# Kernel optimization log

Hardware: AMD Instinct MI355X
Metric: run time of the kernel (lower is better)

The kernel has to match this reference:

```python
import jax, jax.numpy as jnp
import numpy as np

PROJ_DIM = 128
TEMP = 0.1
CLAMP_VAL = 50.0
EPS = 1e-6


def _coords(H, W):
    # [H*W, 2] grid of (x, y) coordinates, matching torch meshgrid indexing='ij'
    xs = jnp.arange(W, dtype=jnp.float32)
    ys = jnp.arange(H, dtype=jnp.float32)
    grid_y, grid_x = jnp.meshgrid(ys, xs, indexing='ij')
    return jnp.stack([grid_x.reshape(-1), grid_y.reshape(-1)], axis=-1)


def setup_inputs() -> dict:
    key = jax.random.key(0)
    k1, k2 = jax.random.split(key)
    B, C, H, W = 2, 128, 96, 96
    fL = jax.random.normal(k1, (B, C, H, W), dtype=jnp.float32)
    fR = jax.random.normal(k2, (B, C, H, W), dtype=jnp.float32)
    return {"fL": fL, "fR": fR}


def reference(fL, fR):
    B, C, H, W = fL.shape
    HW = H * W
    scale = jnp.float32(np.sqrt(PROJ_DIM))

    # L2-normalize over channel dim with epsilon clamp
    fLn = fL / jnp.maximum(jnp.linalg.norm(fL, axis=1, keepdims=True), EPS)
    fRn = fR / jnp.maximum(jnp.linalg.norm(fR, axis=1, keepdims=True), EPS)

    q = fLn.reshape(B, C, HW).transpose(0, 2, 1).astype(jnp.float32)  # [B, HW, C]
    k = fRn.reshape(B, C, HW).astype(jnp.float32)                      # [B, C, HW]

    coords = _coords(H, W)  # [HW, 2]

    # Global correlation: [B, HW, HW] (chunking in the original is math-equivalent)
    corr = jnp.einsum('bqc,bck->bqk', q, k) / scale
    corr = jnp.clip(corr / TEMP, -CLAMP_VAL, CLAMP_VAL)
    prob = jax.nn.softmax(corr, axis=-1)

    expected_pos = prob @ coords                 # [B, HW, 2]
    max_prob = jnp.max(prob, axis=-1)            # [B, HW]

    flow_abs = expected_pos.reshape(B, H, W, 2).transpose(0, 3, 1, 2)  # [B, 2, H, W]
    conf = max_prob.reshape(B, 1, H, W)

    src = coords.reshape(H, W, 2).transpose(2, 0, 1)[None]  # [1, 2, H, W]
    flow = (flow_abs - src).astype(fL.dtype)
    conf = conf.astype(fL.dtype)
    return flow, conf
```

## Files before the change

### kernel.cpp

```cpp
#include <hip/hip_runtime.h>
#include <stdint.h>

#define HW 9216
#define CDIM 128
#define WIDTH 96
#define BATCH 2
#define SPLITS 4
#define KSPLIT 2304
#define NTILE 18

#define QSCALE 0.44194173824159216f
#define MXSCALE 2.8853900817779268f

typedef _Float16 half8 __attribute__((ext_vector_type(8)));
typedef float f32x16 __attribute__((ext_vector_type(16)));
typedef float float4v __attribute__((ext_vector_type(4)));
typedef float float2v __attribute__((ext_vector_type(2)));

__global__ __launch_bounds__(256) void norm_kernel(const float* __restrict__ fL,
                                                   const float* __restrict__ fR,
                                                   _Float16* __restrict__ Qh,
                                                   _Float16* __restrict__ Kh)
{
    __shared__ float ssred[4][64];
    __shared__ _Float16 ot[64 * 130];

    const float* src = (blockIdx.y == 0) ? fL : fR;
    _Float16* dst    = (blockIdx.y == 0) ? Qh : Kh;
    const float outScale = (blockIdx.y == 0) ? QSCALE : 1.0f;

    const int t = threadIdx.x;
    const int pos_l = t & 63, cg = t >> 6;
    const int pos0 = blockIdx.x * 64;
    const int b = pos0 / HW, pos_in = pos0 % HW + pos_l;

    const float* p = src + (size_t)b * CDIM * HW + pos_in;

    float v[32];
    float ss = 0.f;
    #pragma unroll
    for (int j = 0; j < 32; ++j) {
        v[j] = p[(size_t)(cg * 32 + j) * HW];
        ss += v[j] * v[j];
    }
    ssred[cg][pos_l] = ss;
    __syncthreads();
    float tot = ssred[0][pos_l] + ssred[1][pos_l] + ssred[2][pos_l] + ssred[3][pos_l];
    float scale = outScale / fmaxf(sqrtf(tot), 1e-6f);

    #pragma unroll
    for (int j = 0; j < 32; ++j)
        ot[pos_l * 130 + cg * 32 + j] = (_Float16)(v[j] * scale);
    __syncthreads();

    uint4* og = (uint4*)(dst + (size_t)(b * HW + pos0 % HW + 0) * CDIM);
    #pragma unroll
    for (int i = 0; i < 4; ++i) {
        int idx = i * 256 + t;
        int row = idx >> 4, chunk = idx & 15;
        og[idx] = *(const uint4*)&ot[row * 130 + chunk * 8];
    }
}

__global__ __launch_bounds__(512, 4) void attn_kernel(const _Float16* __restrict__ Qh,
                                                      const _Float16* __restrict__ Kh,
                                                      float4* __restrict__ part)
{
    __shared__ __align__(16) _Float16 Ks[2 * 128 * 128];

    const int qt = blockIdx.x, split = blockIdx.y, b = blockIdx.z;
    const int t = threadIdx.x;
    const int lane = t & 63, wave = t >> 6;
    const int wq = wave >> 2, wk = wave & 3;
    const int lane31 = lane & 31, hi = lane >> 5;
    const int ln15 = lane & 15, qd = lane >> 4;

    const char* kp0 = (const char*)(Kh + (size_t)b * HW * CDIM) +
                      (size_t)(split * KSPLIT) * (CDIM * 2);

    int voff[4];
    #pragma unroll
    for (int i = 0; i < 4; ++i) {
        int r = wave * 16 + i * 4 + qd;
        voff[i] = r * 256 + ((ln15 ^ (r & 15)) << 4);
    }

    #define STAGE(TILE, BUF)                                                     \
        {                                                                        \
            const char* kb_ = kp0 + (size_t)(TILE) * 32768;                      \
            _Float16* db_ = &Ks[(BUF) * 16384 + wave * (16 * 128)];              \
            _Pragma("unroll")                                                    \
            for (int i_ = 0; i_ < 4; ++i_)                                       \
                __builtin_amdgcn_global_load_lds(                                \
                    (const __attribute__((address_space(1))) uint32_t*)(kb_ + voff[i_]), \
                    (__attribute__((address_space(3))) uint32_t*)(db_ + i_ * (4 * 128)), \
                    16, 0, 0);                                                   \
        }

    STAGE(0, 0);

    half8 qf[8];
    {
        const char* qb = (const char*)(Qh +
            ((size_t)(b * HW + qt * 64 + wq * 32 + lane31)) * CDIM);
        #pragma unroll
        for (int kc = 0; kc < 8; ++kc)
            qf[kc] = *(const half8*)(qb + kc * 32 + hi * 16);
    }

    int rdoff[8];
    #pragma unroll
    for (int kc = 0; kc < 8; ++kc)
        rdoff[kc] = ((wk * 32 + lane31) << 8) + ((((kc << 1) | hi) ^ ln15) << 4);

    float2v xb2[3], yw2[3];
    #pragma unroll
    for (int p = 0; p < 3; ++p) {
        xb2[p] = (float2v)(float)(32 * ((p + wk) % 3));
        yw2[p] = (float2v)(float)(split * 24 + (4 * p + wk) / 3);
    }

    float2v E2[8];
    #pragma unroll
    for (int p = 0; p < 8; ++p) E2[p] = (float2v)0.f;
    float2v mx2 = (float2v)(-1.0e30f);
    float2v axb2 = (float2v)0.f, ay2 = (float2v)0.f;

    const char* ksb = (const char*)&Ks[0];
    const float2v C4 = (float2v)(1.0f / 24.0f), C3 = (float2v)(1.0f / 6.0f),
                  C2 = (float2v)0.5f, C1 = (float2v)1.0f;

    __syncthreads();

    #pragma unroll
    for (int kt = 0; kt < NTILE; ++kt) {
        const int cur = kt & 1;
        const int ph = kt % 3;
        const float yadd = (float)(4 * (kt / 3));

        if (kt < NTILE - 1) STAGE(kt + 1, 1 - cur);

        f32x16 acc;
        __builtin_amdgcn_s_setprio(1);
        #pragma unroll
        for (int kc = 0; kc < 8; ++kc) {
            half8 kf = *(const half8*)(ksb + cur * 32768 + rdoff[kc]);
            acc = __builtin_amdgcn_mfma_f32_32x32x16_f16(
                kf, qf[kc], (kc == 0) ? (f32x16)0.f : acc, 0, 0, 0);
        }
        __builtin_amdgcn_s_setprio(0);

        float2v lt2;
        #pragma unroll
        for (int p = 0; p < 8; ++p) {
            float2v w;
            w.x = acc[2 * p];
            w.y = acc[2 * p + 1];
            mx2 = __builtin_elementwise_max(mx2, w);
            float2v h = w * C4 + C3;
            h = h * w + C2;
            h = h * w + C1;
            h = h * w + C1;
            float2v e = h * h;
            E2[p] += e;
            lt2 = (p == 0) ? e : (lt2 + e);
        }
        axb2 += lt2 * xb2[ph];
        ay2  += lt2 * (yw2[ph] + (float2v)yadd);
        __syncthreads();
    }

    float l = 0.f, axc = 0.f;
    #pragma unroll
    for (int p = 0; p < 8; ++p) {
        const float c0 = (float)(((2 * p) & 3) + 8 * ((2 * p) >> 2));
        l   += E2[p].x + E2[p].y;
        axc += c0 * E2[p].x + (c0 + 1.0f) * E2[p].y;
    }
    float ax = axc + (float)(4 * hi) * l + axb2.x + axb2.y;
    float ay = ay2.x + ay2.y;
    float mx = fmaxf(mx2.x, mx2.y);

    l  += __shfl_xor(l, 32, 64);
    ax += __shfl_xor(ax, 32, 64);
    ay += __shfl_xor(ay, 32, 64);
    mx  = fmaxf(mx, __shfl_xor(mx, 32, 64));

    if (hi == 0) {
        int row = qt * 64 + wq * 32 + lane31;
        part[(size_t)(split * 4 + wk) * (BATCH * HW) + b * HW + row] =
            make_float4(l, ax, ay, __builtin_amdgcn_exp2f(mx * MXSCALE));
    }
    #undef STAGE
}

__global__ __launch_bounds__(256) void combine_kernel(const float4* __restrict__ part,
                                                      float* __restrict__ out)
{
    int tid = blockIdx.x * 256 + threadIdx.x;
    int b = tid / HW, pos = tid % HW;
    float l = 0.f, ax = 0.f, ay = 0.f, mx = 0.f;
    #pragma unroll
    for (int s = 0; s < 16; ++s) {
        float4 v = part[(size_t)s * (BATCH * HW) + tid];
        l += v.x; ax += v.y; ay += v.z; mx = fmaxf(mx, v.w);
    }
    float inv = 1.0f / l;
    int x = pos % WIDTH, y = pos / WIDTH;
    out[(size_t)b * 2 * HW + pos]           = ax * inv - (float)x;
    out[(size_t)b * 2 * HW + HW + pos]      = ay * inv - (float)y;
    out[(size_t)BATCH * 2 * HW + (size_t)b * HW + pos] = mx * inv;
}

extern "C" void kernel_launch(void* const* d_in, const int* in_sizes, int n_in,
                              void* d_out, int out_size, void* d_ws, size_t ws_size,
                              hipStream_t stream)
{
    const float* fL = (const float*)d_in[0];
    const float* fR = (const float*)d_in[1];
    float* out = (float*)d_out;

    char* ws = (char*)d_ws;
    const size_t QH_BYTES = (size_t)BATCH * HW * CDIM * sizeof(_Float16);
    _Float16* Qh  = (_Float16*)ws;
    _Float16* Kh  = (_Float16*)(ws + QH_BYTES);
    float4*   part = (float4*)(ws + 2 * QH_BYTES);

    norm_kernel<<<dim3((BATCH * HW) / 64, 2), 256, 0, stream>>>(fL, fR, Qh, Kh);
    attn_kernel<<<dim3(HW / 64, SPLITS, BATCH), 512, 0, stream>>>(Qh, Kh, part);
    combine_kernel<<<dim3((BATCH * HW) / 256), 256, 0, stream>>>(part, out);
}
```

Before: 137.5 us.

## Retile attention to 128-query tiles with triple-buffered K and XCD-aware block mapping

The attention kernel now covers 128 query rows per workgroup (4x2 wave grid) over 64-key tiles instead of 64 queries over 128 keys. This halves how often each K tile is streamed per query and the number of partial results the combine step reduces. K staging moves to a 3-buffer ring that prefetches two tiles ahead, with explicit vmcnt waits and a single barrier per tile in place of two __syncthreads. Blocks are remapped across the 8 XCDs by index swizzling, and launch bounds rise to 6 waves per SIMD. The risks are higher register pressure under the tighter bounds, correctness of the hand-written waitcnt pipeline, and smaller MFMA work per barrier.

```diff
diff --git a/kernel.cpp b/kernel.cpp
--- a/kernel.cpp
+++ b/kernel.cpp
@@ -7,14 +7,16 @@
 #define BATCH 2
 #define SPLITS 4
 #define KSPLIT 2304
-#define NTILE 18
+#define NTILE 36
+#define QTILE 128
+#define NQT (HW / QTILE)
+#define NWG (NQT * SPLITS * BATCH)
 
 #define QSCALE 0.44194173824159216f
 #define MXSCALE 2.8853900817779268f
 
 typedef _Float16 half8 __attribute__((ext_vector_type(8)));
 typedef float f32x16 __attribute__((ext_vector_type(16)));
-typedef float float4v __attribute__((ext_vector_type(4)));
 typedef float float2v __attribute__((ext_vector_type(2)));
 
 __global__ __launch_bounds__(256) void norm_kernel(const float* __restrict__ fL,
@@ -62,35 +64,49 @@
     }
 }
 
-__global__ __launch_bounds__(512, 4) void attn_kernel(const _Float16* __restrict__ Qh,
+__global__ __launch_bounds__(512, 6) void attn_kernel(const _Float16* __restrict__ Qh,
                                                       const _Float16* __restrict__ Kh,
                                                       float4* __restrict__ part)
 {
-    __shared__ __align__(16) _Float16 Ks[2 * 128 * 128];
-
-    const int qt = blockIdx.x, split = blockIdx.y, b = blockIdx.z;
+    __shared__ __align__(16) _Float16 Ks[3 * 64 * 128];
+
+    const int wg0 = blockIdx.x;
+    const int nid = (wg0 & 7) * (NWG / 8) + (wg0 >> 3);
+    const int qt = nid % NQT;
+    const int split = (nid / NQT) % SPLITS;
+    const int b = nid / (NQT * SPLITS);
+
     const int t = threadIdx.x;
     const int lane = t & 63, wave = t >> 6;
-    const int wq = wave >> 2, wk = wave & 3;
+    const int wq = wave >> 1, wk = wave & 1;
     const int lane31 = lane & 31, hi = lane >> 5;
     const int ln15 = lane & 15, qd = lane >> 4;
 
     const char* kp0 = (const char*)(Kh + (size_t)b * HW * CDIM) +
                       (size_t)(split * KSPLIT) * (CDIM * 2);
 
-    int voff[4];
-    #pragma unroll
-    for (int i = 0; i < 4; ++i) {
-        int r = wave * 16 + i * 4 + qd;
+    half8 qf[8];
+    {
+        const char* qb = (const char*)(Qh +
+            ((size_t)(b * HW + qt * QTILE + wq * 32 + lane31)) * CDIM);
+        #pragma unroll
+        for (int kc = 0; kc < 8; ++kc)
+            qf[kc] = *(const half8*)(qb + kc * 32 + hi * 16);
+    }
+
+    int voff[2];
+    #pragma unroll
+    for (int i = 0; i < 2; ++i) {
+        int r = wave * 8 + i * 4 + qd;
         voff[i] = r * 256 + ((ln15 ^ (r & 15)) << 4);
     }
 
     #define STAGE(TILE, BUF)                                                     \
         {                                                                        \
-            const char* kb_ = kp0 + (size_t)(TILE) * 32768;                      \
-            _Float16* db_ = &Ks[(BUF) * 16384 + wave * (16 * 128)];              \
+            const char* kb_ = kp0 + (size_t)(TILE) * 16384;                      \
+            _Float16* db_ = &Ks[(BUF) * 8192 + wave * (8 * 128)];                \
             _Pragma("unroll")                                                    \
-            for (int i_ = 0; i_ < 4; ++i_)                                       \
+            for (int i_ = 0; i_ < 2; ++i_)                                       \
                 __builtin_amdgcn_global_load_lds(                                \
                     (const __attribute__((address_space(1))) uint32_t*)(kb_ + voff[i_]), \
                     (__attribute__((address_space(3))) uint32_t*)(db_ + i_ * (4 * 128)), \
@@ -98,26 +114,18 @@
         }
 
     STAGE(0, 0);
-
-    half8 qf[8];
-    {
-        const char* qb = (const char*)(Qh +
-            ((size_t)(b * HW + qt * 64 + wq * 32 + lane31)) * CDIM);
-        #pragma unroll
-        for (int kc = 0; kc < 8; ++kc)
-            qf[kc] = *(const half8*)(qb + kc * 32 + hi * 16);
-    }
+    STAGE(1, 1);
 
     int rdoff[8];
     #pragma unroll
     for (int kc = 0; kc < 8; ++kc)
         rdoff[kc] = ((wk * 32 + lane31) << 8) + ((((kc << 1) | hi) ^ ln15) << 4);
 
-    float2v xb2[3], yw2[3];
+    float xb[3], yw[3];
     #pragma unroll
     for (int p = 0; p < 3; ++p) {
-        xb2[p] = (float2v)(float)(32 * ((p + wk) % 3));
-        yw2[p] = (float2v)(float)(split * 24 + (4 * p + wk) / 3);
+        xb[p] = (float)(32 * ((2 * p + wk) % 3));
+        yw[p] = (float)(split * 24 + (2 * p + wk) / 3);
     }
 
     float2v E2[8];
@@ -130,21 +138,23 @@
     const float2v C4 = (float2v)(1.0f / 24.0f), C3 = (float2v)(1.0f / 6.0f),
                   C2 = (float2v)0.5f, C1 = (float2v)1.0f;
 
-    __syncthreads();
-
     #pragma unroll
     for (int kt = 0; kt < NTILE; ++kt) {
-        const int cur = kt & 1;
-        const int ph = kt % 3;
-        const float yadd = (float)(4 * (kt / 3));
-
-        if (kt < NTILE - 1) STAGE(kt + 1, 1 - cur);
+        const int cur = kt % 3;
+        const float yadd = (float)(2 * (kt / 3));
+
+        __builtin_amdgcn_sched_barrier(0);
+        if (kt < NTILE - 1) asm volatile("s_waitcnt vmcnt(2)" ::: "memory");
+        else                asm volatile("s_waitcnt vmcnt(0)" ::: "memory");
+        __builtin_amdgcn_s_barrier();
+        __builtin_amdgcn_sched_barrier(0);
+        if (kt < NTILE - 2) STAGE(kt + 2, (kt + 2) % 3);
 
         f32x16 acc;
         __builtin_amdgcn_s_setprio(1);
         #pragma unroll
         for (int kc = 0; kc < 8; ++kc) {
-            half8 kf = *(const half8*)(ksb + cur * 32768 + rdoff[kc]);
+            half8 kf = *(const half8*)(ksb + cur * 16384 + rdoff[kc]);
             acc = __builtin_amdgcn_mfma_f32_32x32x16_f16(
                 kf, qf[kc], (kc == 0) ? (f32x16)0.f : acc, 0, 0, 0);
         }
@@ -165,9 +175,8 @@
             E2[p] += e;
             lt2 = (p == 0) ? e : (lt2 + e);
         }
-        axb2 += lt2 * xb2[ph];
-        ay2  += lt2 * (yw2[ph] + (float2v)yadd);
-        __syncthreads();
+        axb2 += lt2 * (float2v)xb[cur];
+        ay2  += lt2 * (float2v)(yw[cur] + yadd);
     }
 
     float l = 0.f, axc = 0.f;
@@ -187,8 +196,8 @@
     mx  = fmaxf(mx, __shfl_xor(mx, 32, 64));
 
     if (hi == 0) {
-        int row = qt * 64 + wq * 32 + lane31;
-        part[(size_t)(split * 4 + wk) * (BATCH * HW) + b * HW + row] =
+        int row = qt * QTILE + wq * 32 + lane31;
+        part[(size_t)(split * 2 + wk) * (BATCH * HW) + b * HW + row] =
             make_float4(l, ax, ay, __builtin_amdgcn_exp2f(mx * MXSCALE));
     }
     #undef STAGE
@@ -201,7 +210,7 @@
     int b = tid / HW, pos = tid % HW;
     float l = 0.f, ax = 0.f, ay = 0.f, mx = 0.f;
     #pragma unroll
-    for (int s = 0; s < 16; ++s) {
+    for (int s = 0; s < 8; ++s) {
         float4 v = part[(size_t)s * (BATCH * HW) + tid];
         l += v.x; ax += v.y; ay += v.z; mx = fmaxf(mx, v.w);
     }
@@ -227,6 +236,6 @@
     float4*   part = (float4*)(ws + 2 * QH_BYTES);
 
     norm_kernel<<<dim3((BATCH * HW) / 64, 2), 256, 0, stream>>>(fL, fR, Qh, Kh);
-    attn_kernel<<<dim3(HW / 64, SPLITS, BATCH), 512, 0, stream>>>(Qh, Kh, part);
+    attn_kernel<<<dim3(NWG), 512, 0, stream>>>(Qh, Kh, part);
     combine_kernel<<<dim3((BATCH * HW) / 256), 256, 0, stream>>>(part, out);
 }
```

New measurement: 348.8 us. 2.54x slower.

## Restructure attention into 256-query tiles over small resident key slices

Applied to the files above, without the earlier changes.

The attention kernel now uses 32 key splits of 288 keys. Each block loads its whole 288-key slice into LDS once, with no double buffering and no per-tile barriers. Each wave handles 64 queries (two 32-row MFMA groups that share each K fragment), blocks are remapped with an XCD-aware swizzle, and the launch becomes a flat 1D grid of 256-thread blocks. The aim is to remove per-tile syncs and reuse K fragments across more queries, at the cost of more register pressure and a larger partials buffer for the combine kernel to reduce (32 splits instead of 16).

```diff
diff --git a/kernel.cpp b/kernel.cpp
--- a/kernel.cpp
+++ b/kernel.cpp
@@ -5,16 +5,18 @@
 #define CDIM 128
 #define WIDTH 96
 #define BATCH 2
-#define SPLITS 4
-#define KSPLIT 2304
-#define NTILE 18
+#define SPLITS 32
+#define KSPLIT 288
+#define NKG 9
+#define QTILE 256
+#define NQT (HW / QTILE)
+#define NWG (NQT * SPLITS * BATCH)
 
 #define QSCALE 0.44194173824159216f
 #define MXSCALE 2.8853900817779268f
 
 typedef _Float16 half8 __attribute__((ext_vector_type(8)));
 typedef float f32x16 __attribute__((ext_vector_type(16)));
-typedef float float4v __attribute__((ext_vector_type(4)));
 typedef float float2v __attribute__((ext_vector_type(2)));
 
 __global__ __launch_bounds__(256) void norm_kernel(const float* __restrict__ fL,
@@ -62,69 +64,74 @@
     }
 }
 
-__global__ __launch_bounds__(512, 4) void attn_kernel(const _Float16* __restrict__ Qh,
+__global__ __launch_bounds__(256, 2) void attn_kernel(const _Float16* __restrict__ Qh,
                                                       const _Float16* __restrict__ Kh,
                                                       float4* __restrict__ part)
 {
-    __shared__ __align__(16) _Float16 Ks[2 * 128 * 128];
-
-    const int qt = blockIdx.x, split = blockIdx.y, b = blockIdx.z;
+    __shared__ __align__(16) _Float16 Ks[KSPLIT * 128];
+
+    const int wg0 = blockIdx.x;
+    const int nid = (wg0 & 7) * (NWG / 8) + (wg0 >> 3);
+    const int qt = nid % NQT;
+    const int sb = nid / NQT;
+    const int split = sb & 31;
+    const int b = sb >> 5;
+
     const int t = threadIdx.x;
     const int lane = t & 63, wave = t >> 6;
-    const int wq = wave >> 2, wk = wave & 3;
     const int lane31 = lane & 31, hi = lane >> 5;
     const int ln15 = lane & 15, qd = lane >> 4;
 
     const char* kp0 = (const char*)(Kh + (size_t)b * HW * CDIM) +
                       (size_t)(split * KSPLIT) * (CDIM * 2);
 
-    int voff[4];
-    #pragma unroll
-    for (int i = 0; i < 4; ++i) {
-        int r = wave * 16 + i * 4 + qd;
-        voff[i] = r * 256 + ((ln15 ^ (r & 15)) << 4);
-    }
-
-    #define STAGE(TILE, BUF)                                                     \
-        {                                                                        \
-            const char* kb_ = kp0 + (size_t)(TILE) * 32768;                      \
-            _Float16* db_ = &Ks[(BUF) * 16384 + wave * (16 * 128)];              \
-            _Pragma("unroll")                                                    \
-            for (int i_ = 0; i_ < 4; ++i_)                                       \
-                __builtin_amdgcn_global_load_lds(                                \
-                    (const __attribute__((address_space(1))) uint32_t*)(kb_ + voff[i_]), \
-                    (__attribute__((address_space(3))) uint32_t*)(db_ + i_ * (4 * 128)), \
-                    16, 0, 0);                                                   \
-        }
-
-    STAGE(0, 0);
-
-    half8 qf[8];
     {
-        const char* qb = (const char*)(Qh +
-            ((size_t)(b * HW + qt * 64 + wq * 32 + lane31)) * CDIM);
-        #pragma unroll
-        for (int kc = 0; kc < 8; ++kc)
-            qf[kc] = *(const half8*)(qb + kc * 32 + hi * 16);
+        int voff4[4];
+        #pragma unroll
+        for (int i = 0; i < 4; ++i) {
+            int r = wave * 72 + i * 4 + qd;
+            voff4[i] = r * 256 + ((ln15 ^ (r & 15)) << 4) - i * 1024;
+        }
+        _Float16* db = &Ks[wave * (72 * 128)];
+        #pragma unroll
+        for (int i = 0; i < 18; ++i)
+            __builtin_amdgcn_global_load_lds(
+                (const __attribute__((address_space(1))) uint32_t*)(kp0 + voff4[i & 3] + i * 1024),
+                (__attribute__((address_space(3))) uint32_t*)(db + i * 512),
+                16, 0, 0);
+    }
+
+    half8 qf[2][8];
+    {
+        #pragma unroll
+        for (int s = 0; s < 2; ++s) {
+            const char* qb = (const char*)(Qh +
+                ((size_t)(b * HW + qt * QTILE + wave * 64 + s * 32 + lane31)) * CDIM);
+            #pragma unroll
+            for (int kc = 0; kc < 8; ++kc)
+                qf[s][kc] = *(const half8*)(qb + kc * 32 + hi * 16);
+        }
     }
 
     int rdoff[8];
     #pragma unroll
     for (int kc = 0; kc < 8; ++kc)
-        rdoff[kc] = ((wk * 32 + lane31) << 8) + ((((kc << 1) | hi) ^ ln15) << 4);
-
-    float2v xb2[3], yw2[3];
-    #pragma unroll
-    for (int p = 0; p < 3; ++p) {
-        xb2[p] = (float2v)(float)(32 * ((p + wk) % 3));
-        yw2[p] = (float2v)(float)(split * 24 + (4 * p + wk) / 3);
-    }
-
-    float2v E2[8];
-    #pragma unroll
-    for (int p = 0; p < 8; ++p) E2[p] = (float2v)0.f;
-    float2v mx2 = (float2v)(-1.0e30f);
-    float2v axb2 = (float2v)0.f, ay2 = (float2v)0.f;
+        rdoff[kc] = (lane31 << 8) + ((((kc << 1) | hi) ^ ln15) << 4);
+
+    const float ysp = (float)(split * 3);
+
+    float2v E2[2][8];
+    #pragma unroll
+    for (int s = 0; s < 2; ++s)
+        #pragma unroll
+        for (int p = 0; p < 8; ++p) E2[s][p] = (float2v)0.f;
+    float2v mx2[2], axb2[2], ay2[2];
+    #pragma unroll
+    for (int s = 0; s < 2; ++s) {
+        mx2[s] = (float2v)(-1.0e30f);
+        axb2[s] = (float2v)0.f;
+        ay2[s] = (float2v)0.f;
+    }
 
     const char* ksb = (const char*)&Ks[0];
     const float2v C4 = (float2v)(1.0f / 24.0f), C3 = (float2v)(1.0f / 6.0f),
@@ -133,65 +140,65 @@
     __syncthreads();
 
     #pragma unroll
-    for (int kt = 0; kt < NTILE; ++kt) {
-        const int cur = kt & 1;
-        const int ph = kt % 3;
-        const float yadd = (float)(4 * (kt / 3));
-
-        if (kt < NTILE - 1) STAGE(kt + 1, 1 - cur);
-
-        f32x16 acc;
-        __builtin_amdgcn_s_setprio(1);
+    for (int kg = 0; kg < NKG; ++kg) {
+        f32x16 acc[2];
         #pragma unroll
         for (int kc = 0; kc < 8; ++kc) {
-            half8 kf = *(const half8*)(ksb + cur * 32768 + rdoff[kc]);
-            acc = __builtin_amdgcn_mfma_f32_32x32x16_f16(
-                kf, qf[kc], (kc == 0) ? (f32x16)0.f : acc, 0, 0, 0);
-        }
-        __builtin_amdgcn_s_setprio(0);
-
-        float2v lt2;
+            half8 kf = *(const half8*)(ksb + kg * 8192 + rdoff[kc]);
+            #pragma unroll
+            for (int s = 0; s < 2; ++s)
+                acc[s] = __builtin_amdgcn_mfma_f32_32x32x16_f16(
+                    kf, qf[s][kc], (kc == 0) ? (f32x16)0.f : acc[s], 0, 0, 0);
+        }
+
+        const float xb = (float)(32 * (kg % 3));
+        const float yk = ysp + (float)(kg / 3);
+        #pragma unroll
+        for (int s = 0; s < 2; ++s) {
+            float2v lt2;
+            #pragma unroll
+            for (int p = 0; p < 8; ++p) {
+                float2v w;
+                w.x = acc[s][2 * p];
+                w.y = acc[s][2 * p + 1];
+                mx2[s] = __builtin_elementwise_max(mx2[s], w);
+                float2v h = w * C4 + C3;
+                h = h * w + C2;
+                h = h * w + C1;
+                h = h * w + C1;
+                float2v e = h * h;
+                E2[s][p] += e;
+                lt2 = (p == 0) ? e : (lt2 + e);
+            }
+            axb2[s] += lt2 * (float2v)xb;
+            ay2[s]  += lt2 * (float2v)yk;
+        }
+    }
+
+    #pragma unroll
+    for (int s = 0; s < 2; ++s) {
+        float l = 0.f, axc = 0.f;
         #pragma unroll
         for (int p = 0; p < 8; ++p) {
-            float2v w;
-            w.x = acc[2 * p];
-            w.y = acc[2 * p + 1];
-            mx2 = __builtin_elementwise_max(mx2, w);
-            float2v h = w * C4 + C3;
-            h = h * w + C2;
-            h = h * w + C1;
-            h = h * w + C1;
-            float2v e = h * h;
-            E2[p] += e;
-            lt2 = (p == 0) ? e : (lt2 + e);
-        }
-        axb2 += lt2 * xb2[ph];
-        ay2  += lt2 * (yw2[ph] + (float2v)yadd);
-        __syncthreads();
-    }
-
-    float l = 0.f, axc = 0.f;
-    #pragma unroll
-    for (int p = 0; p < 8; ++p) {
-        const float c0 = (float)(((2 * p) & 3) + 8 * ((2 * p) >> 2));
-        l   += E2[p].x + E2[p].y;
-        axc += c0 * E2[p].x + (c0 + 1.0f) * E2[p].y;
-    }
-    float ax = axc + (float)(4 * hi) * l + axb2.x + axb2.y;
-    float ay = ay2.x + ay2.y;
-    float mx = fmaxf(mx2.x, mx2.y);
-
-    l  += __shfl_xor(l, 32, 64);
-    ax += __shfl_xor(ax, 32, 64);
-    ay += __shfl_xor(ay, 32, 64);
-    mx  = fmaxf(mx, __shfl_xor(mx, 32, 64));
-
-    if (hi == 0) {
-        int row = qt * 64 + wq * 32 + lane31;
-        part[(size_t)(split * 4 + wk) * (BATCH * HW) + b * HW + row] =
-            make_float4(l, ax, ay, __builtin_amdgcn_exp2f(mx * MXSCALE));
-    }
-    #undef STAGE
+            const float c0 = (float)(((2 * p) & 3) + 8 * ((2 * p) >> 2));
+            l   += E2[s][p].x + E2[s][p].y;
+            axc += c0 * E2[s][p].x + (c0 + 1.0f) * E2[s][p].y;
+        }
+        float ax = axc + (float)(4 * hi) * l + axb2[s].x + axb2[s].y;
+        float ay = ay2[s].x + ay2[s].y;
+        float mx = fmaxf(mx2[s].x, mx2[s].y);
+
+        l  += __shfl_xor(l, 32, 64);
+        ax += __shfl_xor(ax, 32, 64);
+        ay += __shfl_xor(ay, 32, 64);
+        mx  = fmaxf(mx, __shfl_xor(mx, 32, 64));
+
+        if (hi == 0) {
+            int row = qt * QTILE + wave * 64 + s * 32 + lane31;
+            part[(size_t)split * (BATCH * HW) + b * HW + row] =
+                make_float4(l, ax, ay, __builtin_amdgcn_exp2f(mx * MXSCALE));
+        }
+    }
 }
 
 __global__ __launch_bounds__(256) void combine_kernel(const float4* __restrict__ part,
@@ -201,7 +208,7 @@
     int b = tid / HW, pos = tid % HW;
     float l = 0.f, ax = 0.f, ay = 0.f, mx = 0.f;
     #pragma unroll
-    for (int s = 0; s < 16; ++s) {
+    for (int s = 0; s < SPLITS; ++s) {
         float4 v = part[(size_t)s * (BATCH * HW) + tid];
         l += v.x; ax += v.y; ay += v.z; mx = fmaxf(mx, v.w);
     }
@@ -227,6 +234,6 @@
     float4*   part = (float4*)(ws + 2 * QH_BYTES);
 
     norm_kernel<<<dim3((BATCH * HW) / 64, 2), 256, 0, stream>>>(fL, fR, Qh, Kh);
-    attn_kernel<<<dim3(HW / 64, SPLITS, BATCH), 512, 0, stream>>>(Qh, Kh, part);
+    attn_kernel<<<dim3(NWG), 256, 0, stream>>>(Qh, Kh, part);
     combine_kernel<<<dim3((BATCH * HW) / 256), 256, 0, stream>>>(part, out);
 }
```

New measurement: 132.3 us. 1.04x faster.
